# Optimization experiments

Measured on AMD Instinct MI355X. Metric: run time of the kernel, lower is better.

Reference implementation:

```python
import jax, jax.numpy as jnp
import numpy as np

N = 262144      # nodes
C = 64          # in_channels
K = 16          # neighbors per node
NUM_CLASSES = 40


def setup_inputs() -> dict:
    key = jax.random.key(0)
    ks = jax.random.split(key, 8)
    x = jax.random.normal(ks[0], (N, C), dtype=jnp.float32)
    nbr_idx = jax.random.randint(ks[1], (N, K), 0, N, dtype=jnp.int64)
    # CPE: depthwise 1D conv, kernel 3, per-channel weights [C,3] + bias [C]
    cpe_w = jax.random.normal(ks[2], (C, 3), dtype=jnp.float32) * (1.0 / np.sqrt(3.0))
    cpe_b = jnp.zeros((C,), dtype=jnp.float32)
    # Grapher: max-relative graph conv projection [2C -> C]
    g_w = jax.random.normal(ks[3], (2 * C, C), dtype=jnp.float32) * (1.0 / np.sqrt(2.0 * C))
    g_b = jnp.zeros((C,), dtype=jnp.float32)
    # classifier head [C -> NUM_CLASSES]
    o_w = jax.random.normal(ks[4], (C, NUM_CLASSES), dtype=jnp.float32) * (1.0 / np.sqrt(C))
    o_b = jnp.zeros((NUM_CLASSES,), dtype=jnp.float32)
    return {"x": x, "nbr_idx": nbr_idx, "cpe_w": cpe_w, "cpe_b": cpe_b,
            "g_w": g_w, "g_b": g_b, "o_w": o_w, "o_b": o_b}


def reference(x, nbr_idx, cpe_w, cpe_b, g_w, g_b, o_w, o_b):
    # --- CPE: depthwise conv1d (kernel 3, pad 1, groups=C) + residual ---
    xp = jnp.pad(x, ((1, 1), (0, 0)))  # [N+2, C]
    conv = (xp[:-2] * cpe_w[:, 0] + xp[1:-1] * cpe_w[:, 1] + xp[2:] * cpe_w[:, 2]) + cpe_b
    h = x + conv  # [N, C]
    # --- Grapher: max-relative graph conv over precomputed kNN + residual ---
    xj = h[nbr_idx]                          # [N, K, C] irregular gather
    rel = jnp.max(xj - h[:, None, :], axis=1)  # [N, C] max-relative features
    feat = jnp.concatenate([h, rel], axis=-1)  # [N, 2C]
    h = h + (feat @ g_w + g_b)                 # [N, C]
    # --- head + log_softmax over classes (dim=1) ---
    logits = h @ o_w + o_b                     # [N, NUM_CLASSES]
    return jax.nn.log_softmax(logits, axis=1)
```

## Files before the change

kernel.cpp:

```cpp
#include <hip/hip_runtime.h>
#include <hip/hip_bf16.h>

#define N_NODES 262144
#define C_CH 64
#define K_NBR 16
#define NCLS 40

typedef unsigned short ushort_t;
typedef __attribute__((ext_vector_type(8))) short short8;
typedef __attribute__((ext_vector_type(4))) float floatx4;

__device__ __forceinline__ float bu2f(ushort_t u) {
    union { unsigned u32; float f; } v; v.u32 = ((unsigned)u) << 16; return v.f;
}
__device__ __forceinline__ ushort_t f2bu(float f) {
    union { float f; unsigned u; } v; v.f = f;
    unsigned r = v.u + 0x7FFFu + ((v.u >> 16) & 1u);
    return (ushort_t)(r >> 16);
}
__device__ __forceinline__ floatx4 bcast4(float g) {
    floatx4 v; v[0] = g; v[1] = g; v[2] = g; v[3] = g; return v;
}
__device__ __forceinline__ int ldi(const int* p, long i)       { return p[i]; }
__device__ __forceinline__ int ldi(const long long* p, long i) { return (int)p[i]; }

__global__ void cpe_kernel(const float* __restrict__ x,
                           const float* __restrict__ cw,
                           const float* __restrict__ cb,
                           ushort_t* __restrict__ h,
                           const void* __restrict__ nbr,
                           int* __restrict__ flags) {
    if (blockIdx.x == 0 && threadIdx.x < 64) {
        int lane = threadIdx.x;
        const int* ni = (const int*)nbr;
        bool zodd = (ni[2 * lane + 1] == 0);
        unsigned long long mz = __ballot(zodd);
        if (lane == 0) flags[1] = (mz == ~0ULL) ? 1 : 0;
    }
    int t  = blockIdx.x * 256 + threadIdx.x;
    int ig = t >> 4;
    int cq = t & 15;
    int i0 = ig << 2;
    int c0 = cq * 4;
    float w0[4], w1[4], w2[4], bb[4];
#pragma unroll
    for (int j = 0; j < 4; ++j) {
        w0[j] = cw[(c0 + j) * 3 + 0];
        w1[j] = cw[(c0 + j) * 3 + 1];
        w2[j] = cw[(c0 + j) * 3 + 2];
        bb[j] = cb[c0 + j];
    }
    float4 v[6];
#pragma unroll
    for (int r = 0; r < 6; ++r) {
        int i = i0 - 1 + r;
        if (i >= 0 && i < N_NODES) v[r] = *(const float4*)(x + (size_t)i * C_CH + c0);
        else                       v[r] = make_float4(0.f, 0.f, 0.f, 0.f);
    }
#pragma unroll
    for (int j = 0; j < 4; ++j) {
        float a[4] = {v[j].x, v[j].y, v[j].z, v[j].w};
        float b[4] = {v[j+1].x, v[j+1].y, v[j+1].z, v[j+1].w};
        float c[4] = {v[j+2].x, v[j+2].y, v[j+2].z, v[j+2].w};
        unsigned p0 = 0, p1 = 0;
#pragma unroll
        for (int q = 0; q < 4; ++q) {
            float r = b[q] + bb[q];
            r = fmaf(a[q], w0[q], r);
            r = fmaf(b[q], w1[q], r);
            r = fmaf(c[q], w2[q], r);
            unsigned u = (unsigned)f2bu(r);
            if (q < 2) p0 |= u << (q * 16);
            else       p1 |= u << ((q - 2) * 16);
        }
        *(uint2*)(h + (size_t)(i0 + j) * C_CH + c0) = make_uint2(p0, p1);
    }
}

template <typename IT>
__device__ __forceinline__ void fused_body(const ushort_t* __restrict__ hws,
                                           const IT* __restrict__ nbr,
                                           const float* __restrict__ gb,
                                           const float* __restrict__ ob,
                                           float* __restrict__ out,
                                           const ushort_t* sWt,
                                           const ushort_t* sOt,
                                           ushort_t* feat,
                                           int lane) {
    const int lanelo = lane & 15;
    const int quad   = lane >> 4;
    float gbf[4];
#pragma unroll
    for (int nt = 0; nt < 4; ++nt) gbf[nt] = gb[nt * 16 + lanelo];
    float obf[3];
#pragma unroll
    for (int nt = 0; nt < 3; ++nt) {
        int n = nt * 16 + lanelo;
        obf[nt] = (n < NCLS) ? ob[n] : 0.f;
    }
    const bool ok2 = (lanelo < 8);

    const int nTasks = N_NODES / 16;
    const int wslots = gridDim.x * 8;
    const int wv     = threadIdx.x >> 6;

    for (int task0 = blockIdx.x * 8 + wv; task0 < nTasks; task0 += wslots) {
        const int task = __builtin_amdgcn_readfirstlane(task0);
        const int nb0  = task * 16;
        const IT* nrow = nbr + (size_t)nb0 * K_NBR;

        for (int t = 0; t < 16; ++t) {
            float v[16];
#pragma unroll
            for (int k = 0; k < 16; ++k) {
                int idx = (int)nrow[t * K_NBR + k];
                v[k] = bu2f(hws[((size_t)(unsigned)idx << 6) + lane]);
            }
#pragma unroll
            for (int s = 8; s; s >>= 1)
#pragma unroll
                for (int k = 0; k < s; ++k)
                    v[k] = fmaxf(v[k], v[k + s]);
            ushort_t hu = hws[((size_t)(unsigned)(nb0 + t) << 6) + lane];
            feat[t * 136 + lane]      = hu;
            feat[t * 136 + 64 + lane] = f2bu(v[0] - bu2f(hu));
        }
        asm volatile("" ::: "memory");

        floatx4 acc[4];
#pragma unroll
        for (int nt = 0; nt < 4; ++nt) acc[nt] = bcast4(gbf[nt]);
#pragma unroll
        for (int s = 0; s < 4; ++s) {
            short8 af = *(const short8*)(feat + lanelo * 136 + s * 32 + quad * 8);
#pragma unroll
            for (int nt = 0; nt < 4; ++nt) {
                short8 bf = *(const short8*)(sWt + (nt * 16 + lanelo) * 136 + s * 32 + quad * 8);
                acc[nt] = __builtin_amdgcn_mfma_f32_16x16x32_bf16(af, bf, acc[nt], 0, 0, 0);
            }
        }

        ushort_t* h2w = feat;
#pragma unroll
        for (int nt = 0; nt < 4; ++nt)
#pragma unroll
            for (int r = 0; r < 4; ++r)
                h2w[(quad * 4 + r) * 88 + nt * 16 + lanelo] = f2bu(acc[nt][r]);
        asm volatile("" ::: "memory");

        floatx4 accH[3];
#pragma unroll
        for (int nt = 0; nt < 3; ++nt) accH[nt] = bcast4(obf[nt]);
#pragma unroll
        for (int s = 0; s < 2; ++s) {
            short8 hf = *(const short8*)(h2w + lanelo * 88 + s * 32 + quad * 8);
#pragma unroll
            for (int nt = 0; nt < 3; ++nt) {
                short8 bf = *(const short8*)(sOt + (nt * 16 + lanelo) * 72 + s * 32 + quad * 8);
                accH[nt] = __builtin_amdgcn_mfma_f32_16x16x32_bf16(hf, bf, accH[nt], 0, 0, 0);
            }
        }
        asm volatile("" ::: "memory");

        float* fOut = (float*)feat;
#pragma unroll
        for (int r = 0; r < 4; ++r) {
            float v0 = accH[0][r], v1 = accH[1][r];
            float v2 = ok2 ? accH[2][r] : -1e30f;
            float m = fmaxf(fmaxf(v0, v1), v2);
#pragma unroll
            for (int off = 1; off < 16; off <<= 1) m = fmaxf(m, __shfl_xor(m, off, 64));
            float s = __expf(v0 - m) + __expf(v1 - m) + (ok2 ? __expf(v2 - m) : 0.f);
#pragma unroll
            for (int off = 1; off < 16; off <<= 1) s += __shfl_xor(s, off, 64);
            float li = m + __logf(s);
            int rowbase = (quad * 4 + r) * NCLS;
            fOut[rowbase + lanelo]      = v0 - li;
            fOut[rowbase + 16 + lanelo] = v1 - li;
            if (ok2) fOut[rowbase + 32 + lanelo] = v2 - li;
        }
        asm volatile("" ::: "memory");

        float* obase = out + (size_t)nb0 * NCLS;
#pragma unroll
        for (int k = 0; k < 10; ++k)
            obase[k * 64 + lane] = fOut[k * 64 + lane];
        asm volatile("" ::: "memory");
    }
}

__global__ void __launch_bounds__(512, 4)
fused_kernel(const int* __restrict__ flags,
             const ushort_t* __restrict__ hws,
             const void* __restrict__ nbrv,
             const float* __restrict__ gw,
             const float* __restrict__ gb,
             const float* __restrict__ ow,
             const float* __restrict__ ob,
             float* __restrict__ out) {
    __shared__ __align__(16) ushort_t sWt[64 * 136];
    __shared__ __align__(16) ushort_t sOt[48 * 72];
    __shared__ __align__(16) ushort_t sFeatU[8][2176];

    for (int t = threadIdx.x; t < 64 * 128 / 4; t += 512) {
        int k  = t >> 4;
        int n0 = (t & 15) * 4;
        float4 w4 = *(const float4*)(gw + k * C_CH + n0);
        float wv4[4] = {w4.x, w4.y, w4.z, w4.w};
#pragma unroll
        for (int q = 0; q < 4; ++q) {
            float w = wv4[q];
            if (k == n0 + q) w += 1.0f;
            sWt[(n0 + q) * 136 + k] = f2bu(w);
        }
    }
    for (int t = threadIdx.x; t < 48 * 64; t += 512) {
        int n = t >> 6, k = t & 63;
        float w = (n < NCLS) ? ow[k * NCLS + n] : 0.f;
        sOt[n * 72 + k] = f2bu(w);
    }
    __syncthreads();

    const int lane = threadIdx.x & 63;
    const int wv   = __builtin_amdgcn_readfirstlane(threadIdx.x >> 6);
    ushort_t* feat = &sFeatU[wv][0];

    if (flags[1]) fused_body<long long>(hws, (const long long*)nbrv, gb, ob, out, sWt, sOt, feat, lane);
    else          fused_body<int>      (hws, (const int*)nbrv,       gb, ob, out, sWt, sOt, feat, lane);
}

template <typename IT>
__global__ void __launch_bounds__(256, 4)
graph_head_kernel(const int* __restrict__ flags,
                  const ushort_t* __restrict__ hws,
                  const IT* __restrict__ nbr,
                  const float* __restrict__ gw,
                  const float* __restrict__ gb,
                  const float* __restrict__ ow,
                  const float* __restrict__ ob,
                  float* __restrict__ out) {
    if ((flags[1] != 0) != (sizeof(IT) == 8)) return;

    __shared__ __align__(16) ushort_t sWt[64 * 136];
    __shared__ __align__(16) ushort_t sOt[48 * 72];
    __shared__ __align__(16) ushort_t sFeat[4][16 * 136];
    __shared__ __align__(16) ushort_t sH2[4][16 * 88];

    for (int t = threadIdx.x; t < 64 * 128 / 4; t += 256) {
        int k  = t >> 4;
        int n0 = (t & 15) * 4;
        float4 w4 = *(const float4*)(gw + k * C_CH + n0);
        float wv4[4] = {w4.x, w4.y, w4.z, w4.w};
#pragma unroll
        for (int q = 0; q < 4; ++q) {
            float w = wv4[q];
            if (k == n0 + q) w += 1.0f;
            sWt[(n0 + q) * 136 + k] = f2bu(w);
        }
    }
    for (int t = threadIdx.x; t < 48 * 64; t += 256) {
        int n = t >> 6, k = t & 63;
        float w = (n < NCLS) ? ow[k * NCLS + n] : 0.f;
        sOt[n * 72 + k] = f2bu(w);
    }
    __syncthreads();

    const int lane   = threadIdx.x & 63;
    const int wave   = threadIdx.x >> 6;
    const int lanelo = lane & 15;
    const int quad   = lane >> 4;

    float gbf[4];
#pragma unroll
    for (int nt = 0; nt < 4; ++nt) gbf[nt] = gb[nt * 16 + lanelo];
    float obf[3];
#pragma unroll
    for (int nt = 0; nt < 3; ++nt) {
        int n = nt * 16 + lanelo;
        obf[nt] = (n < NCLS) ? ob[n] : 0.f;
    }
    const bool ok2 = (lanelo < 8);

    for (int g = blockIdx.x; g < (N_NODES >> 6); g += gridDim.x) {
        const int nb0 = g * 64 + wave * 16;
        ushort_t* h2w = &sH2[wave][0];
        ushort_t* feat = &sFeat[wave][0];

        floatx4 acc[4];
#pragma unroll
        for (int nt = 0; nt < 4; ++nt) acc[nt] = bcast4(gbf[nt]);

#pragma unroll
        for (int q = 0; q < 4; ++q) {
            int idxv = ldi(nbr, (long)nb0 * K_NBR + q * 64 + lane);
#pragma unroll
            for (int tt = 0; tt < 4; ++tt) {
                int t = q * 4 + tt;
                ushort_t hu = hws[(size_t)(nb0 + t) * C_CH + lane];
                float hif = bu2f(hu);
                float mx = -1e30f;
#pragma unroll
                for (int k = 0; k < 16; ++k) {
                    int j = __shfl(idxv, tt * 16 + k, 64);
                    mx = fmaxf(mx, bu2f(hws[((size_t)(unsigned)j << 6) + lane]));
                }
                feat[t * 136 + lane]      = hu;
                feat[t * 136 + 64 + lane] = f2bu(mx - hif);
            }
        }
        __syncthreads();
#pragma unroll
        for (int s = 0; s < 4; ++s) {
            short8 af = *(const short8*)(feat + lanelo * 136 + s * 32 + quad * 8);
#pragma unroll
            for (int nt = 0; nt < 4; ++nt) {
                short8 bf = *(const short8*)(sWt + (nt * 16 + lanelo) * 136 + s * 32 + quad * 8);
                acc[nt] = __builtin_amdgcn_mfma_f32_16x16x32_bf16(af, bf, acc[nt], 0, 0, 0);
            }
        }

#pragma unroll
        for (int nt = 0; nt < 4; ++nt)
#pragma unroll
            for (int r = 0; r < 4; ++r)
                h2w[(quad * 4 + r) * 88 + nt * 16 + lanelo] = f2bu(acc[nt][r]);
        __syncthreads();

        floatx4 accH[3];
#pragma unroll
        for (int nt = 0; nt < 3; ++nt) accH[nt] = bcast4(obf[nt]);
#pragma unroll
        for (int s = 0; s < 2; ++s) {
            short8 hf = *(const short8*)(h2w + lanelo * 88 + s * 32 + quad * 8);
#pragma unroll
            for (int nt = 0; nt < 3; ++nt) {
                short8 bf = *(const short8*)(sOt + (nt * 16 + lanelo) * 72 + s * 32 + quad * 8);
                accH[nt] = __builtin_amdgcn_mfma_f32_16x16x32_bf16(hf, bf, accH[nt], 0, 0, 0);
            }
        }

        float* fOut = (float*)h2w;
#pragma unroll
        for (int r = 0; r < 4; ++r) {
            float v0 = accH[0][r], v1 = accH[1][r];
            float v2 = ok2 ? accH[2][r] : -1e30f;
            float m = fmaxf(fmaxf(v0, v1), v2);
#pragma unroll
            for (int off = 1; off < 16; off <<= 1) m = fmaxf(m, __shfl_xor(m, off, 64));
            float s = __expf(v0 - m) + __expf(v1 - m) + (ok2 ? __expf(v2 - m) : 0.f);
#pragma unroll
            for (int off = 1; off < 16; off <<= 1) s += __shfl_xor(s, off, 64);
            float li = m + __logf(s);
            int rowbase = (quad * 4 + r) * NCLS;
            fOut[rowbase + lanelo]      = v0 - li;
            fOut[rowbase + 16 + lanelo] = v1 - li;
            if (ok2) fOut[rowbase + 32 + lanelo] = v2 - li;
        }
        __syncthreads();

        float* obase = out + (size_t)nb0 * NCLS;
#pragma unroll
        for (int k = 0; k < 10; ++k)
            obase[k * 64 + lane] = fOut[k * 64 + lane];
    }
}

extern "C" void kernel_launch(void* const* d_in, const int* in_sizes, int n_in,
                              void* d_out, int out_size, void* d_ws, size_t ws_size,
                              hipStream_t stream) {
    const float* x  = (const float*)d_in[0];
    const float* cw = (const float*)d_in[2];
    const float* cb = (const float*)d_in[3];
    const float* gw = (const float*)d_in[4];
    const float* gb = (const float*)d_in[5];
    const float* ow = (const float*)d_in[6];
    const float* ob = (const float*)d_in[7];
    float* out = (float*)d_out;

    int* flags = (int*)d_ws;
    ushort_t* hws = (ushort_t*)((char*)d_ws + 1024);

    const bool fits = (ws_size >= (size_t)(1024 + 33554432ULL));

    cpe_kernel<<<(N_NODES / 4 * 16) / 256, 256, 0, stream>>>(x, cw, cb, hws,
                                                             d_in[1], flags);
    if (fits) {
        fused_kernel<<<512, 512, 0, stream>>>(flags, hws, d_in[1],
                                              gw, gb, ow, ob, out);
    } else {
        graph_head_kernel<int><<<2048, 256, 0, stream>>>(
            flags, hws, (const int*)d_in[1], gw, gb, ow, ob, out);
        graph_head_kernel<long long><<<2048, 256, 0, stream>>>(
            flags, hws, (const long long*)d_in[1], gw, gb, ow, ob, out);
    }
}
```

Before: 214.6 us.

## Gather neighbors directly into MFMA operand layout, dropping shared feature staging

The fused kernel's gather stage now has each lane own one node row and load 16-byte bf16 vectors for that node and its neighbors, matching the MFMA A-operand layout. This replaces the old scheme where each wavefront processed nodes one at a time, did scalar per-channel loads, and staged features through shared memory. That removes the feature LDS buffer and its write/read round trip and issues wider, more independent gather loads. Shared memory per block shrinks, so launch bounds and grid size are raised toward 6 blocks per CU. The trade-off is more registers per lane (16 indices plus 16 running maxima), which may limit occupancy, and only 16 of the 64 lanes are distinct rows per gather.

After: 254.2 us. 1.18x slower.

```diff
diff --git a/kernel.cpp b/kernel.cpp
--- a/kernel.cpp
+++ b/kernel.cpp
@@ -85,10 +85,11 @@
                                            float* __restrict__ out,
                                            const ushort_t* sWt,
                                            const ushort_t* sOt,
-                                           ushort_t* feat,
+                                           ushort_t* h2w,
                                            int lane) {
     const int lanelo = lane & 15;
     const int quad   = lane >> 4;
+    const int qc     = quad * 8;
     float gbf[4];
 #pragma unroll
     for (int nt = 0; nt < 4; ++nt) gbf[nt] = gb[nt * 16 + lanelo];
@@ -104,35 +105,55 @@
     const int wslots = gridDim.x * 8;
     const int wv     = threadIdx.x >> 6;
 
-    for (int task0 = blockIdx.x * 8 + wv; task0 < nTasks; task0 += wslots) {
-        const int task = __builtin_amdgcn_readfirstlane(task0);
-        const int nb0  = task * 16;
-        const IT* nrow = nbr + (size_t)nb0 * K_NBR;
-
-        for (int t = 0; t < 16; ++t) {
-            float v[16];
-#pragma unroll
-            for (int k = 0; k < 16; ++k) {
-                int idx = (int)nrow[t * K_NBR + k];
-                v[k] = bu2f(hws[((size_t)(unsigned)idx << 6) + lane]);
-            }
-#pragma unroll
-            for (int s = 8; s; s >>= 1)
-#pragma unroll
-                for (int k = 0; k < s; ++k)
-                    v[k] = fmaxf(v[k], v[k + s]);
-            ushort_t hu = hws[((size_t)(unsigned)(nb0 + t) << 6) + lane];
-            feat[t * 136 + lane]      = hu;
-            feat[t * 136 + 64 + lane] = f2bu(v[0] - bu2f(hu));
-        }
-        asm volatile("" ::: "memory");
+    for (int task = blockIdx.x * 8 + wv; task < nTasks; task += wslots) {
+        const int nb0 = task * 16;
+        const int myn = nb0 + lanelo;
+
+        const ushort_t* hrow = hws + ((size_t)(unsigned)myn << 6);
+        short8 af0 = *(const short8*)(hrow + qc);
+        short8 af1 = *(const short8*)(hrow + 32 + qc);
+
+        int idx[16];
+        const IT* nrow = nbr + (size_t)(unsigned)myn * K_NBR;
+#pragma unroll
+        for (int j = 0; j < 16; ++j) idx[j] = (int)nrow[j];
+
+        float vmx[16];
+        {
+            const ushort_t* np = hws + ((size_t)(unsigned)idx[0] << 6);
+            short8 n0 = *(const short8*)(np + qc);
+            short8 n1 = *(const short8*)(np + 32 + qc);
+#pragma unroll
+            for (int e = 0; e < 8; ++e) {
+                vmx[e]     = bu2f((ushort_t)n0[e]);
+                vmx[8 + e] = bu2f((ushort_t)n1[e]);
+            }
+        }
+#pragma unroll
+        for (int j = 1; j < 16; ++j) {
+            const ushort_t* np = hws + ((size_t)(unsigned)idx[j] << 6);
+            short8 n0 = *(const short8*)(np + qc);
+            short8 n1 = *(const short8*)(np + 32 + qc);
+#pragma unroll
+            for (int e = 0; e < 8; ++e) {
+                vmx[e]     = fmaxf(vmx[e],     bu2f((ushort_t)n0[e]));
+                vmx[8 + e] = fmaxf(vmx[8 + e], bu2f((ushort_t)n1[e]));
+            }
+        }
+
+        short8 af2, af3;
+#pragma unroll
+        for (int e = 0; e < 8; ++e) {
+            af2[e] = (short)f2bu(vmx[e]     - bu2f((ushort_t)af0[e]));
+            af3[e] = (short)f2bu(vmx[8 + e] - bu2f((ushort_t)af1[e]));
+        }
 
         floatx4 acc[4];
 #pragma unroll
         for (int nt = 0; nt < 4; ++nt) acc[nt] = bcast4(gbf[nt]);
 #pragma unroll
         for (int s = 0; s < 4; ++s) {
-            short8 af = *(const short8*)(feat + lanelo * 136 + s * 32 + quad * 8);
+            short8 af = (s == 0) ? af0 : (s == 1) ? af1 : (s == 2) ? af2 : af3;
 #pragma unroll
             for (int nt = 0; nt < 4; ++nt) {
                 short8 bf = *(const short8*)(sWt + (nt * 16 + lanelo) * 136 + s * 32 + quad * 8);
@@ -140,7 +161,6 @@
             }
         }
 
-        ushort_t* h2w = feat;
 #pragma unroll
         for (int nt = 0; nt < 4; ++nt)
 #pragma unroll
@@ -162,7 +182,7 @@
         }
         asm volatile("" ::: "memory");
 
-        float* fOut = (float*)feat;
+        float* fOut = (float*)h2w;
 #pragma unroll
         for (int r = 0; r < 4; ++r) {
             float v0 = accH[0][r], v1 = accH[1][r];
@@ -189,7 +209,7 @@
     }
 }
 
-__global__ void __launch_bounds__(512, 4)
+__global__ void __launch_bounds__(512, 6)
 fused_kernel(const int* __restrict__ flags,
              const ushort_t* __restrict__ hws,
              const void* __restrict__ nbrv,
@@ -200,7 +220,7 @@
              float* __restrict__ out) {
     __shared__ __align__(16) ushort_t sWt[64 * 136];
     __shared__ __align__(16) ushort_t sOt[48 * 72];
-    __shared__ __align__(16) ushort_t sFeatU[8][2176];
+    __shared__ __align__(16) ushort_t sH2[8][16 * 88];
 
     for (int t = threadIdx.x; t < 64 * 128 / 4; t += 512) {
         int k  = t >> 4;
@@ -223,10 +243,10 @@
 
     const int lane = threadIdx.x & 63;
     const int wv   = __builtin_amdgcn_readfirstlane(threadIdx.x >> 6);
-    ushort_t* feat = &sFeatU[wv][0];
-
-    if (flags[1]) fused_body<long long>(hws, (const long long*)nbrv, gb, ob, out, sWt, sOt, feat, lane);
-    else          fused_body<int>      (hws, (const int*)nbrv,       gb, ob, out, sWt, sOt, feat, lane);
+    ushort_t* h2w  = &sH2[wv][0];
+
+    if (flags[1]) fused_body<long long>(hws, (const long long*)nbrv, gb, ob, out, sWt, sOt, h2w, lane);
+    else          fused_body<int>      (hws, (const int*)nbrv,       gb, ob, out, sWt, sOt, h2w, lane);
 }
 
 template <typename IT>
@@ -385,7 +405,7 @@
     cpe_kernel<<<(N_NODES / 4 * 16) / 256, 256, 0, stream>>>(x, cw, cb, hws,
                                                              d_in[1], flags);
     if (fits) {
-        fused_kernel<<<512, 512, 0, stream>>>(flags, hws, d_in[1],
+        fused_kernel<<<768, 512, 0, stream>>>(flags, hws, d_in[1],
                                               gw, gb, ow, ob, out);
     } else {
         graph_head_kernel<int><<<2048, 256, 0, stream>>>(
```
